# Optimization experiments

Measured on AMD Instinct MI355X. Metric: run time of the kernel, lower is better.

## Reference

```python
import jax, jax.numpy as jnp
import numpy as np

E = 100000      # number of edges
MUL = 64        # multiplicity of each irrep (0e and 1o)
DIM = MUL * 1 + MUL * 3  # 256 feature dim for 64x0e + 64x1o

INV_SQRT3 = 1.0 / np.sqrt(3.0)          # wigner-3j value for (0,1,1) and (1,1,0) paths
ALPHA0 = 1.0 / np.sqrt(2.0 * MUL * MUL)  # path norm: 2 paths feed the 0e output
ALPHA1 = 1.0 / np.sqrt(2.0 * MUL * MUL)  # path norm: 2 paths feed the 1o output


def _split(t):
    # t: [E, 256] -> scalars [E, MUL], vectors [E, MUL, 3]
    s = t[:, :MUL]
    v = t[:, MUL:].reshape(-1, MUL, 3)
    return s, v


def fc_tensor_product(x, y, W000, W110, W011, W101):
    """FullyConnectedTensorProduct(64x0e+64x1o, 64x0e+64x1o -> 64x0e+64x1o).

    Paths (uvw-connected, one weight [MUL,MUL,MUL] each):
      (0e,0e)->0e : cg = 1
      (1o,1o)->0e : cg = delta_ij / sqrt(3)
      (0e,1o)->1o : cg = delta_jk / sqrt(3)
      (1o,0e)->1o : cg = delta_ik / sqrt(3)
    """
    x0, x1 = _split(x)
    y0, y1 = _split(y)
    out0 = ALPHA0 * (
        jnp.einsum('eu,ev,uvw->ew', x0, y0, W000)
        + INV_SQRT3 * jnp.einsum('eui,evi,uvw->ew', x1, y1, W110)
    )
    out1 = ALPHA1 * INV_SQRT3 * (
        jnp.einsum('eu,evi,uvw->ewi', x0, y1, W011)
        + jnp.einsum('eui,ev,uvw->ewi', x1, y0, W101)
    )
    return jnp.concatenate([out0, out1.reshape(-1, MUL * 3)], axis=1)


def setup_inputs() -> dict:
    key = jax.random.key(0)
    ks = jax.random.split(key, 12)
    mk = lambda k, shape: jax.random.normal(k, shape, dtype=jnp.float32)
    return {
        'e1x': mk(ks[0], (E, DIM)),
        'e1y': mk(ks[1], (E, DIM)),
        'e2x': mk(ks[2], (E, DIM)),
        'e2y': mk(ks[3], (E, DIM)),
        'W1_000': mk(ks[4], (MUL, MUL, MUL)),
        'W1_110': mk(ks[5], (MUL, MUL, MUL)),
        'W1_011': mk(ks[6], (MUL, MUL, MUL)),
        'W1_101': mk(ks[7], (MUL, MUL, MUL)),
        'W2_000': mk(ks[8], (MUL, MUL, MUL)),
        'W2_110': mk(ks[9], (MUL, MUL, MUL)),
        'W2_011': mk(ks[10], (MUL, MUL, MUL)),
        'W2_101': mk(ks[11], (MUL, MUL, MUL)),
    }


def reference(e1x, e1y, e2x, e2y,
              W1_000, W1_110, W1_011, W1_101,
              W2_000, W2_110, W2_011, W2_101) -> jnp.ndarray:
    # SimpleEdgeBlock.forward: sum of one fully-connected TP per input tuple
    out = fc_tensor_product(e1x, e1y, W1_000, W1_110, W1_011, W1_101)
    out = out + fc_tensor_product(e2x, e2y, W2_000, W2_110, W2_011, W2_101)
    return out
```

## Files before the change

### kernel.cpp

```cpp
#include <hip/hip_runtime.h>
#include <stdint.h>


typedef __attribute__((ext_vector_type(8))) short short8;
typedef __attribute__((ext_vector_type(16))) float f32x16;
typedef unsigned short u16;

#define ETOT 100000

__device__ __forceinline__ unsigned pk2(float lo, float hi) {
  return __builtin_amdgcn_perm(__builtin_bit_cast(unsigned, hi),
                               __builtin_bit_cast(unsigned, lo), 0x07060302u);
}
__device__ __forceinline__ float bf2f(u16 s) {
  return __builtin_bit_cast(float, ((unsigned)s) << 16);
}
__device__ __forceinline__ void unpk8(short8 s, float f[8]) {
  uint4 u = __builtin_bit_cast(uint4, s);
  unsigned a[4] = {u.x, u.y, u.z, u.w};
#pragma unroll
  for (int jj = 0; jj < 4; ++jj) {
    f[2 * jj]     = __builtin_bit_cast(float, a[jj] << 16);
    f[2 * jj + 1] = __builtin_bit_cast(float, a[jj] & 0xffff0000u);
  }
}
__device__ __forceinline__ short8 scalepack(const float f[8], float ysc) {
  unsigned p0 = pk2(f[0] * ysc, f[1] * ysc);
  unsigned p1 = pk2(f[2] * ysc, f[3] * ysc);
  unsigned p2 = pk2(f[4] * ysc, f[5] * ysc);
  unsigned p3 = pk2(f[6] * ysc, f[7] * ysc);
  uint4 r = make_uint4(p0, p1, p2, p3);
  return __builtin_bit_cast(short8, r);
}
__device__ __forceinline__ short8 pack8(const float f[8]) {
  unsigned p0 = pk2(f[0], f[1]);
  unsigned p1 = pk2(f[2], f[3]);
  unsigned p2 = pk2(f[4], f[5]);
  unsigned p3 = pk2(f[6], f[7]);
  uint4 r = make_uint4(p0, p1, p2, p3);
  return __builtin_bit_cast(short8, r);
}

__global__ void prep_B(const float* __restrict__ W10, const float* __restrict__ W11,
                       const float* __restrict__ W12, const float* __restrict__ W13,
                       const float* __restrict__ W20, const float* __restrict__ W21,
                       const float* __restrict__ W22, const float* __restrict__ W23,
                       u16* __restrict__ B) {
  int idx = blockIdx.x * 256 + threadIdx.x;
  int k = idx & 16383;
  int w = (idx >> 14) & 63;
  int t = idx >> 20;
  int p = k >> 13;
  int half = (k >> 12) & 1;
  int v = (k >> 6) & 63;
  int u = k & 63;
  const float a0 = 0.011048543456039806f;
  const float a0s3 = a0 * 0.5773502691896258f;
  const float* Wsrc;
  float scale;
  if (t == 0) {
    Wsrc = half ? (p ? W21 : W11) : (p ? W20 : W10);
    scale = half ? a0s3 : a0;
  } else {
    Wsrc = half ? (p ? W23 : W13) : (p ? W22 : W12);
    scale = a0s3;
  }
  float val = Wsrc[u * 4096 + v * 64 + w] * scale;
  unsigned ub = __builtin_bit_cast(unsigned, val);
  ub += 0x7fffu + ((ub >> 16) & 1u);
  B[idx] = (u16)(ub >> 16);
}

__global__ __launch_bounds__(128, 2)
void tp_main(const float* __restrict__ e1x, const float* __restrict__ e1y,
             const float* __restrict__ e2x, const float* __restrict__ e2y,
             const u16* __restrict__ B, float* __restrict__ out) {
  __shared__ u16 ylds[4 * 64 * 64];
  __shared__ u16 blds[2][2 * 4 * 64 * 8];

  const int tid = threadIdx.x;
  const int wave = tid >> 6;
  const int lane = tid & 63;
  const int m = lane & 31;
  const int hw = lane >> 5;
  const int be0 = blockIdx.x * 64;
  const int e0 = be0 + wave * 32;
  const bool active = (e0 < ETOT);
  const int e = e0 + m;

  f32x16 acc[4][2] = {};
  short8 xc[4][4];

  int buf = 0;
#pragma unroll 1
  for (int p = 0; p < 2; ++p) {
    const float* X = p ? e2x : e1x;
    const float* Y = p ? e2y : e1y;
    __syncthreads();

#pragma unroll 4
    for (int n = 0; n < 32; ++n) {
      int flat4 = n * 128 + tid;
      int r = flat4 >> 6;
      int c4 = flat4 & 63;
      if (be0 + r < ETOT) {
        float4 v4 = *(const float4*)(Y + (size_t)(be0 + r) * 256 + c4 * 4);
        float vv[4] = {v4.x, v4.y, v4.z, v4.w};
#pragma unroll
        for (int kk = 0; kk < 4; ++kk) {
          int d = c4 * 4 + kk;
          int ch, vi;
          if (d < 64) { ch = 0; vi = d; }
          else { int dd = d - 64; ch = 1 + dd % 3; vi = dd / 3; }
          ylds[(ch * 64 + vi) * 64 + r] =
              (u16)(__builtin_bit_cast(unsigned, vv[kk]) >> 16);
        }
      }
    }

    if (active) {
#pragma unroll
      for (int q = 0; q < 4; ++q) {
        const float* px = X + (size_t)e * 256 + q * 16 + hw * 8;
        float4 a4 = *(const float4*)px;
        float4 b4 = *(const float4*)(px + 4);
        float f[8] = {a4.x, a4.y, a4.z, a4.w, b4.x, b4.y, b4.z, b4.w};
        xc[0][q] = pack8(f);
      }
#pragma unroll
      for (int i = 0; i < 3; ++i) {
        const float* px = X + (size_t)e * 256 + 64 + i;
#pragma unroll
        for (int q = 0; q < 4; ++q) {
          float f[8];
#pragma unroll
          for (int j = 0; j < 8; ++j) f[j] = px[(q * 16 + hw * 8 + j) * 3];
          xc[1 + i][q] = pack8(f);
        }
      }
    }

    auto stageB = [&](int kk0, int dstbuf) {
#pragma unroll
      for (int q = 0; q < 4; ++q) {
        int flat = q * 128 + tid;
        int t = flat >> 8;
        int kq = (flat >> 6) & 3;
        int w = flat & 63;
        const uint4* g = (const uint4*)(B + (size_t)(t * 64 + w) * 16384 +
                                        p * 8192 + kk0 + kq * 8);
        *(uint4*)&blds[dstbuf][flat * 8] = *g;
      }
    };

    stageB(0, buf);
    __syncthreads();

#pragma unroll 1
    for (int s = 0; s < 256; ++s) {
      if (s < 255) stageB((s + 1) * 32, buf ^ 1);
      if (active) {
        const u16* bb = blds[buf];
#pragma unroll
        for (int ksub = 0; ksub < 2; ++ksub) {
          int kk = s * 32 + ksub * 16;
          int half = kk >> 12;
          int lv = (kk >> 6) & 63;
          int qx = (kk >> 4) & 3;
          float ys[4];
#pragma unroll
          for (int ch = 0; ch < 4; ++ch)
            ys[ch] = bf2f(ylds[(ch * 64 + lv) * 64 + wave * 32 + m]);
          short8 bfrag[2][2];
#pragma unroll
          for (int tb = 0; tb < 2; ++tb)
#pragma unroll
            for (int n = 0; n < 2; ++n) {
              int slot = tb * 256 + (ksub * 2 + hw) * 64 + n * 32 + m;
              bfrag[tb][n] = *(const short8*)&bb[slot * 8];
            }
          short8 af[4];
          if (half == 0) {
            float xf[8];
            unpk8(xc[0][qx], xf);
            af[0] = scalepack(xf, ys[0]);
            af[1] = scalepack(xf, ys[1]);
            af[2] = scalepack(xf, ys[2]);
            af[3] = scalepack(xf, ys[3]);
          } else {
            float x0f[8], x1f[8], x2f[8];
            unpk8(xc[1][qx], x0f);
            unpk8(xc[2][qx], x1f);
            unpk8(xc[3][qx], x2f);
            float z[8];
#pragma unroll
            for (int j = 0; j < 8; ++j)
              z[j] = x0f[j] * ys[1] + x1f[j] * ys[2] + x2f[j] * ys[3];
            af[0] = pack8(z);
            af[1] = scalepack(x0f, ys[0]);
            af[2] = scalepack(x1f, ys[0]);
            af[3] = scalepack(x2f, ys[0]);
          }
#pragma unroll
          for (int t = 0; t < 4; ++t) {
            const int tb = t ? 1 : 0;
            acc[t][0] = __builtin_amdgcn_mfma_f32_32x32x16_bf16(
                af[t], bfrag[tb][0], acc[t][0], 0, 0, 0);
            acc[t][1] = __builtin_amdgcn_mfma_f32_32x32x16_bf16(
                af[t], bfrag[tb][1], acc[t][1], 0, 0, 0);
          }
        }
      }
      __syncthreads();
      buf ^= 1;
    }
  }

  if (active) {
#pragma unroll
    for (int t = 0; t < 4; ++t)
#pragma unroll
      for (int n0 = 0; n0 < 2; ++n0) {
        f32x16 c = acc[t][n0];
        int n = n0 * 32 + m;
#pragma unroll
        for (int r = 0; r < 16; ++r) {
          int row = (r & 3) + 8 * (r >> 2) + 4 * hw;
          int ee = e0 + row;
          size_t off;
          if (t == 0) off = (size_t)ee * 256 + n;
          else        off = (size_t)ee * 256 + 64 + n * 3 + (t - 1);
          out[off] = c[r];
        }
      }
  }
}

extern "C" void kernel_launch(void* const* d_in, const int* in_sizes, int n_in,
                              void* d_out, int out_size, void* d_ws, size_t ws_size,
                              hipStream_t stream) {
  const float* e1x = (const float*)d_in[0];
  const float* e1y = (const float*)d_in[1];
  const float* e2x = (const float*)d_in[2];
  const float* e2y = (const float*)d_in[3];
  const size_t bElems = (size_t)2 * 64 * 16384;
  if (ws_size < bElems * sizeof(u16)) return;
  u16* B = (u16*)d_ws;
  prep_B<<<8192, 256, 0, stream>>>(
      (const float*)d_in[4], (const float*)d_in[5], (const float*)d_in[6],
      (const float*)d_in[7], (const float*)d_in[8], (const float*)d_in[9],
      (const float*)d_in[10], (const float*)d_in[11], B);
  tp_main<<<(ETOT + 63) / 64, 128, 0, stream>>>(e1x, e1y, e2x, e2y, B,
                                                (float*)d_out);
}
```

Baseline: 2.909 ms.

## Stream B and Y tiles via async global-to-LDS DMA with larger k-steps

Swaps the register-staged B copy and the upfront Y transpose into LDS for direct global_load_lds transfers, issued one step ahead and gated by explicit vmcnt waits and raw barriers. The B workspace layout is reordered so each step covers 64 k-values (a full u block for one v and half), and Y scalars for the current v are fetched per step as fp32 instead of bf16. MFMA sections get a raised scheduling priority. The aim is to overlap memory traffic with compute and cut VGPR staging and barrier overhead. In exchange it depends on hand-counted waitcnt values, and the per-step 4-byte Y gathers are strided.

```diff
diff --git a/kernel.cpp b/kernel.cpp
--- a/kernel.cpp
+++ b/kernel.cpp
@@ -11,9 +11,6 @@
 __device__ __forceinline__ unsigned pk2(float lo, float hi) {
   return __builtin_amdgcn_perm(__builtin_bit_cast(unsigned, hi),
                                __builtin_bit_cast(unsigned, lo), 0x07060302u);
-}
-__device__ __forceinline__ float bf2f(u16 s) {
-  return __builtin_bit_cast(float, ((unsigned)s) << 16);
 }
 __device__ __forceinline__ void unpk8(short8 s, float f[8]) {
   uint4 u = __builtin_bit_cast(uint4, s);
@@ -41,19 +38,34 @@
   return __builtin_bit_cast(short8, r);
 }
 
+__device__ __forceinline__ void dma16(const void* g, void* l) {
+  __builtin_amdgcn_global_load_lds(
+      (const __attribute__((address_space(1))) unsigned*)g,
+      (__attribute__((address_space(3))) unsigned*)l, 16, 0, 0);
+}
+__device__ __forceinline__ void dma4(const void* g, void* l) {
+  __builtin_amdgcn_global_load_lds(
+      (const __attribute__((address_space(1))) unsigned*)g,
+      (__attribute__((address_space(3))) unsigned*)l, 4, 0, 0);
+}
+
 __global__ void prep_B(const float* __restrict__ W10, const float* __restrict__ W11,
                        const float* __restrict__ W12, const float* __restrict__ W13,
                        const float* __restrict__ W20, const float* __restrict__ W21,
                        const float* __restrict__ W22, const float* __restrict__ W23,
                        u16* __restrict__ B) {
   int idx = blockIdx.x * 256 + threadIdx.x;
-  int k = idx & 16383;
-  int w = (idx >> 14) & 63;
-  int t = idx >> 20;
-  int p = k >> 13;
-  int half = (k >> 12) & 1;
-  int v = (k >> 6) & 63;
-  int u = k & 63;
+  int j = idx & 7;
+  int w = (idx >> 3) & 63;
+  int oct = (idx >> 9) & 7;
+  int t = (idx >> 12) & 1;
+  int s = idx >> 13;
+  int klin = s * 64 + oct * 8 + j;
+  int p = klin >> 13;
+  int r = klin & 8191;
+  int v = (r >> 7) & 63;
+  int half = (r >> 6) & 1;
+  int u = r & 63;
   const float a0 = 0.011048543456039806f;
   const float a0s3 = a0 * 0.5773502691896258f;
   const float* Wsrc;
@@ -75,48 +87,51 @@
 void tp_main(const float* __restrict__ e1x, const float* __restrict__ e1y,
              const float* __restrict__ e2x, const float* __restrict__ e2y,
              const u16* __restrict__ B, float* __restrict__ out) {
-  __shared__ u16 ylds[4 * 64 * 64];
-  __shared__ u16 blds[2][2 * 4 * 64 * 8];
+  __shared__ u16 blds[2][8192];
+  __shared__ float yv[2][256];
 
   const int tid = threadIdx.x;
-  const int wave = tid >> 6;
+  const int wv = tid >> 6;
   const int lane = tid & 63;
   const int m = lane & 31;
   const int hw = lane >> 5;
   const int be0 = blockIdx.x * 64;
-  const int e0 = be0 + wave * 32;
+  const int e0 = be0 + wv * 32;
   const bool active = (e0 < ETOT);
   const int e = e0 + m;
 
   f32x16 acc[4][2] = {};
   short8 xc[4][4];
 
-  int buf = 0;
+  auto issueB = [&](int s1) {
+    const int cb = s1 * 1024 + wv * 512;
+    const u16* src = B + (size_t)(cb + lane) * 8;
+    u16* dst = (u16*)&blds[s1 & 1][(wv * 512) * 8];
+#pragma unroll
+    for (int q = 0; q < 8; ++q) dma16(src + q * 64 * 8, dst + q * 64 * 8);
+  };
+  auto issueY = [&](int g) {
+    const int b2 = g & 1;
+    if (g > 127) g = 127;
+    const float* Ysrc = (g >> 6) ? e2y : e1y;
+    const int v = g & 63;
+#pragma unroll
+    for (int q = 0; q < 2; ++q) {
+      int f = wv * 128 + q * 64 + lane;
+      int el = f >> 2, ch = f & 3;
+      int eg = be0 + el;
+      if (eg > ETOT - 1) eg = ETOT - 1;
+      const float* src = Ysrc + (size_t)eg * 256 + (ch == 0 ? v : 64 + v * 3 + (ch - 1));
+      dma4(src, &yv[b2][wv * 128 + q * 64]);
+    }
+  };
+
+  issueY(0);
+  issueB(0);
+
 #pragma unroll 1
   for (int p = 0; p < 2; ++p) {
     const float* X = p ? e2x : e1x;
-    const float* Y = p ? e2y : e1y;
-    __syncthreads();
-
-#pragma unroll 4
-    for (int n = 0; n < 32; ++n) {
-      int flat4 = n * 128 + tid;
-      int r = flat4 >> 6;
-      int c4 = flat4 & 63;
-      if (be0 + r < ETOT) {
-        float4 v4 = *(const float4*)(Y + (size_t)(be0 + r) * 256 + c4 * 4);
-        float vv[4] = {v4.x, v4.y, v4.z, v4.w};
-#pragma unroll
-        for (int kk = 0; kk < 4; ++kk) {
-          int d = c4 * 4 + kk;
-          int ch, vi;
-          if (d < 64) { ch = 0; vi = d; }
-          else { int dd = d - 64; ch = 1 + dd % 3; vi = dd / 3; }
-          ylds[(ch * 64 + vi) * 64 + r] =
-              (u16)(__builtin_bit_cast(unsigned, vv[kk]) >> 16);
-        }
-      }
-    }
 
     if (active) {
 #pragma unroll
@@ -140,67 +155,52 @@
       }
     }
 
-    auto stageB = [&](int kk0, int dstbuf) {
-#pragma unroll
-      for (int q = 0; q < 4; ++q) {
-        int flat = q * 128 + tid;
-        int t = flat >> 8;
-        int kq = (flat >> 6) & 3;
-        int w = flat & 63;
-        const uint4* g = (const uint4*)(B + (size_t)(t * 64 + w) * 16384 +
-                                        p * 8192 + kk0 + kq * 8);
-        *(uint4*)&blds[dstbuf][flat * 8] = *g;
-      }
-    };
-
-    stageB(0, buf);
-    __syncthreads();
-
 #pragma unroll 1
-    for (int s = 0; s < 256; ++s) {
-      if (s < 255) stageB((s + 1) * 32, buf ^ 1);
+    for (int sl = 0; sl < 128; ++sl) {
+      const int s = p * 128 + sl;
+      issueB(s + 1 > 255 ? 255 : s + 1);
+      if (!(s & 1)) issueY((s >> 1) + 1);
+      asm volatile("s_waitcnt vmcnt(10)" ::: "memory");
+      __builtin_amdgcn_sched_barrier(0);
+      __builtin_amdgcn_s_barrier();
+
+      const int h = s & 1;
+      const int g = s >> 1;
+      const u16* bb = blds[s & 1];
       if (active) {
-        const u16* bb = blds[buf];
-#pragma unroll
-        for (int ksub = 0; ksub < 2; ++ksub) {
-          int kk = s * 32 + ksub * 16;
-          int half = kk >> 12;
-          int lv = (kk >> 6) & 63;
-          int qx = (kk >> 4) & 3;
-          float ys[4];
-#pragma unroll
-          for (int ch = 0; ch < 4; ++ch)
-            ys[ch] = bf2f(ylds[(ch * 64 + lv) * 64 + wave * 32 + m]);
+        float4 ysv = *(const float4*)&yv[g & 1][(wv * 32 + m) * 4];
+#pragma unroll
+        for (int uq = 0; uq < 4; ++uq) {
           short8 bfrag[2][2];
 #pragma unroll
           for (int tb = 0; tb < 2; ++tb)
 #pragma unroll
-            for (int n = 0; n < 2; ++n) {
-              int slot = tb * 256 + (ksub * 2 + hw) * 64 + n * 32 + m;
-              bfrag[tb][n] = *(const short8*)&bb[slot * 8];
-            }
+            for (int n = 0; n < 2; ++n)
+              bfrag[tb][n] =
+                  *(const short8*)&bb[(tb * 512 + (uq * 2 + hw) * 64 + n * 32 + m) * 8];
           short8 af[4];
-          if (half == 0) {
+          if (h == 0) {
             float xf[8];
-            unpk8(xc[0][qx], xf);
-            af[0] = scalepack(xf, ys[0]);
-            af[1] = scalepack(xf, ys[1]);
-            af[2] = scalepack(xf, ys[2]);
-            af[3] = scalepack(xf, ys[3]);
+            unpk8(xc[0][uq], xf);
+            af[0] = scalepack(xf, ysv.x);
+            af[1] = scalepack(xf, ysv.y);
+            af[2] = scalepack(xf, ysv.z);
+            af[3] = scalepack(xf, ysv.w);
           } else {
             float x0f[8], x1f[8], x2f[8];
-            unpk8(xc[1][qx], x0f);
-            unpk8(xc[2][qx], x1f);
-            unpk8(xc[3][qx], x2f);
+            unpk8(xc[1][uq], x0f);
+            unpk8(xc[2][uq], x1f);
+            unpk8(xc[3][uq], x2f);
             float z[8];
 #pragma unroll
             for (int j = 0; j < 8; ++j)
-              z[j] = x0f[j] * ys[1] + x1f[j] * ys[2] + x2f[j] * ys[3];
+              z[j] = x0f[j] * ysv.y + x1f[j] * ysv.z + x2f[j] * ysv.w;
             af[0] = pack8(z);
-            af[1] = scalepack(x0f, ys[0]);
-            af[2] = scalepack(x1f, ys[0]);
-            af[3] = scalepack(x2f, ys[0]);
+            af[1] = scalepack(x0f, ysv.x);
+            af[2] = scalepack(x1f, ysv.x);
+            af[3] = scalepack(x2f, ysv.x);
           }
+          __builtin_amdgcn_s_setprio(1);
 #pragma unroll
           for (int t = 0; t < 4; ++t) {
             const int tb = t ? 1 : 0;
@@ -209,10 +209,12 @@
             acc[t][1] = __builtin_amdgcn_mfma_f32_32x32x16_bf16(
                 af[t], bfrag[tb][1], acc[t][1], 0, 0, 0);
           }
+          __builtin_amdgcn_s_setprio(0);
         }
       }
-      __syncthreads();
-      buf ^= 1;
+      asm volatile("s_waitcnt lgkmcnt(0)" ::: "memory");
+      __builtin_amdgcn_sched_barrier(0);
+      __builtin_amdgcn_s_barrier();
     }
   }
 
```

New measurement: 2.765 ms. 1.05x faster.
